# Optimization experiments

Measured on AMD Instinct MI355X. Metric: run time of the kernel, lower is better.

## Reference

```python
import jax, jax.numpy as jnp
import numpy as np

BITS_W = 2  # WAGE default weight bitwidth


def _scale(bits):
    return 2.0 ** (bits - 1)


def quantize_w(x):
    """WAGE Quantize.W: clip to [-1+delta, 1-delta], round to grid of step delta,
    with straight-through estimator for gradients."""
    s = _scale(BITS_W)
    delta = 1.0 / s
    xc = jnp.clip(x, -1.0 + delta, 1.0 - delta)
    y = jnp.round(xc * s) / s
    # straight-through: forward uses y, gradient flows as identity to x
    return x + jax.lax.stop_gradient(y - x)


def setup_inputs() -> dict:
    key = jax.random.key(0)
    k1, k2 = jax.random.split(key)
    B, D_IN, C_OUT = 16384, 1024, 1024
    inputs = jax.random.normal(k1, (B, D_IN), dtype=jnp.float32)
    # learned kernel per build(): shape [d_in, c_out]
    kernel = jax.random.normal(k2, (D_IN, C_OUT), dtype=jnp.float32) * 0.5
    return {"inputs": inputs, "kernel": kernel}


def reference(inputs, kernel):
    # quantize weights every forward pass, then dense matmul
    return jnp.matmul(inputs, quantize_w(kernel))
```

## Files before the change

kernel.cpp:

```cpp
#include <hip/hip_runtime.h>

typedef unsigned short u16;
typedef unsigned int u32;

typedef __bf16 bf16x8 __attribute__((ext_vector_type(8)));
typedef float floatx4 __attribute__((ext_vector_type(4)));


__device__ __forceinline__ u32 f2bf(float f) {
    u32 u = __builtin_bit_cast(u32, f);
    return (u + 0x7fffu + ((u >> 16) & 1u)) >> 16;
}

__device__ __forceinline__ float quant_w(float x) {
    float xc = fminf(fmaxf(x, -0.5f), 0.5f);
    return rintf(xc * 2.0f) * 0.5f;
}

__device__ __forceinline__ void gload_lds16(const u16* g, u16* l) {
    __builtin_amdgcn_global_load_lds(
        (const __attribute__((address_space(1))) void*)g,
        (__attribute__((address_space(3))) void*)l,
        16, 0, 0);
}


__global__ __launch_bounds__(256) void cast_a_kernel(const float4* __restrict__ in,
                                                     uint4* __restrict__ out) {
    int t = blockIdx.x * 256 + threadIdx.x;
    float4 a = in[2 * t];
    float4 b = in[2 * t + 1];
    uint4 o;
    o.x = f2bf(a.x) | (f2bf(a.y) << 16);
    o.y = f2bf(a.z) | (f2bf(a.w) << 16);
    o.z = f2bf(b.x) | (f2bf(b.y) << 16);
    o.w = f2bf(b.z) | (f2bf(b.w) << 16);
    out[t] = o;
}


__global__ __launch_bounds__(256) void quant_transpose_kernel(const float* __restrict__ W,
                                                              u16* __restrict__ Bt) {
    __shared__ u16 tile[32][33];
    const int KN = 1024;
    int tx = threadIdx.x;
    int ty = threadIdx.y;
    int k0 = blockIdx.y * 32;
    int n0 = blockIdx.x * 32;
#pragma unroll
    for (int i = 0; i < 4; i++) {
        int kl = ty + i * 8;
        float x = W[(k0 + kl) * KN + n0 + tx];
        tile[kl][tx] = (u16)f2bf(quant_w(x));
    }
    __syncthreads();
#pragma unroll
    for (int i = 0; i < 4; i++) {
        int nl = ty + i * 8;
        Bt[(n0 + nl) * KN + k0 + tx] = tile[tx][nl];
    }
}


__global__ __launch_bounds__(256) void gemm_bt_kernel(const u16* __restrict__ A,
                                                      const u16* __restrict__ Bt,
                                                      float* __restrict__ C) {
    const int K = 1024;
    const int N = 1024;

    __shared__ alignas(16) u16 As[128 * 64];
    __shared__ alignas(16) u16 Bs[128 * 64];

    const int tid = threadIdx.x;
    const int mbase = blockIdx.x * 128;
    const int nbase = blockIdx.y * 128;
    const int lane = tid & 63;
    const int wv = tid >> 6;
    const int wm = (wv & 1) * 64;
    const int wn = (wv >> 1) * 64;
    const int frow = lane & 15;
    const int fkc = lane >> 4;
    const int rsw = frow & 7;

    floatx4 acc[4][4] = {};

    const int srow = tid >> 3;
    const int g8 = (tid & 7) ^ (srow & 7);
    const u16* Aga[4];
    const u16* Bga[4];
#pragma unroll
    for (int q = 0; q < 4; q++) {
        Aga[q] = &A[(size_t)(mbase + q * 32 + srow) * K + g8 * 8];
        Bga[q] = &Bt[(size_t)(nbase + q * 32 + srow) * K + g8 * 8];
    }

    for (int kt = 0; kt < K; kt += 64) {
        __syncthreads();
#pragma unroll
        for (int q = 0; q < 4; q++) {
            gload_lds16(Aga[q] + kt, &As[(q * 256 + tid) * 8]);
            gload_lds16(Bga[q] + kt, &Bs[(q * 256 + tid) * 8]);
        }
        __syncthreads();

#pragma unroll
        for (int s = 0; s < 2; s++) {
            bf16x8 af[4], bf[4];
#pragma unroll
            for (int i = 0; i < 4; i++)
                af[i] = *(const bf16x8*)&As[(wm + i * 16 + frow) * 64 +
                                            (((s * 4 + fkc) ^ rsw) * 8)];
#pragma unroll
            for (int j = 0; j < 4; j++)
                bf[j] = *(const bf16x8*)&Bs[(wn + j * 16 + frow) * 64 +
                                            (((s * 4 + fkc) ^ rsw) * 8)];
#pragma unroll
            for (int i = 0; i < 4; i++)
#pragma unroll
                for (int j = 0; j < 4; j++)
                    acc[i][j] = __builtin_amdgcn_mfma_f32_16x16x32_bf16(
                        af[i], bf[j], acc[i][j], 0, 0, 0);
        }
    }

    const int crow = (lane >> 4) * 4;
    const int ccol = lane & 15;
#pragma unroll
    for (int i = 0; i < 4; i++) {
#pragma unroll
        for (int j = 0; j < 4; j++) {
            float* cp = &C[(size_t)(mbase + wm + i * 16 + crow) * N + nbase + wn + j * 16 + ccol];
#pragma unroll
            for (int r = 0; r < 4; r++) cp[r * N] = acc[i][j][r];
        }
    }
}


extern "C" void kernel_launch(void* const* d_in, const int* in_sizes, int n_in,
                              void* d_out, int out_size, void* d_ws, size_t ws_size,
                              hipStream_t stream) {
    const float* A = (const float*)d_in[0];
    const float* W = (const float*)d_in[1];
    float* C = (float*)d_out;

    u16* Abf = (u16*)d_ws;
    u16* Btq = (u16*)((char*)d_ws + (size_t)33554432);

    cast_a_kernel<<<8192, 256, 0, stream>>>((const float4*)A, (uint4*)Abf);
    quant_transpose_kernel<<<dim3(32, 32), dim3(32, 8), 0, stream>>>(W, Btq);
    gemm_bt_kernel<<<dim3(128, 8), 256, 0, stream>>>(Abf, Btq, C);
}
```

Before: 151.0 us.

## Fuse fp32-to-bf16 cast of A into GEMM tile load

Drops the separate cast kernel that wrote a bf16 copy of A. The GEMM now reads fp32 A directly, converts it with a packed bf16 convert instruction, and writes the swizzled LDS tile through registers. This removes a launch plus the write and re-read of a 32 MB intermediate. In exchange A is loaded synchronously through VGPRs rather than asynchronously into LDS, and each A element is re-read and re-converted by all 8 N-blocks, doubling A traffic from L2/HBM.

```diff
diff --git a/kernel.cpp b/kernel.cpp
--- a/kernel.cpp
+++ b/kernel.cpp
@@ -17,25 +17,17 @@
     return rintf(xc * 2.0f) * 0.5f;
 }
 
+__device__ __forceinline__ u32 cvt_pk_bf16(float lo, float hi) {
+    u32 r;
+    asm("v_cvt_pk_bf16_f32 %0, %1, %2" : "=v"(r) : "v"(lo), "v"(hi));
+    return r;
+}
+
 __device__ __forceinline__ void gload_lds16(const u16* g, u16* l) {
     __builtin_amdgcn_global_load_lds(
         (const __attribute__((address_space(1))) void*)g,
         (__attribute__((address_space(3))) void*)l,
         16, 0, 0);
-}
-
-
-__global__ __launch_bounds__(256) void cast_a_kernel(const float4* __restrict__ in,
-                                                     uint4* __restrict__ out) {
-    int t = blockIdx.x * 256 + threadIdx.x;
-    float4 a = in[2 * t];
-    float4 b = in[2 * t + 1];
-    uint4 o;
-    o.x = f2bf(a.x) | (f2bf(a.y) << 16);
-    o.y = f2bf(a.z) | (f2bf(a.w) << 16);
-    o.z = f2bf(b.x) | (f2bf(b.y) << 16);
-    o.w = f2bf(b.z) | (f2bf(b.w) << 16);
-    out[t] = o;
 }
 
 
@@ -62,9 +54,9 @@
 }
 
 
-__global__ __launch_bounds__(256) void gemm_bt_kernel(const u16* __restrict__ A,
-                                                      const u16* __restrict__ Bt,
-                                                      float* __restrict__ C) {
+__global__ __launch_bounds__(256) void gemm_fused_kernel(const float* __restrict__ A32,
+                                                         const u16* __restrict__ Bt,
+                                                         float* __restrict__ C) {
     const int K = 1024;
     const int N = 1024;
 
@@ -86,21 +78,40 @@
 
     const int srow = tid >> 3;
     const int g8 = (tid & 7) ^ (srow & 7);
-    const u16* Aga[4];
     const u16* Bga[4];
 #pragma unroll
-    for (int q = 0; q < 4; q++) {
-        Aga[q] = &A[(size_t)(mbase + q * 32 + srow) * K + g8 * 8];
+    for (int q = 0; q < 4; q++)
         Bga[q] = &Bt[(size_t)(nbase + q * 32 + srow) * K + g8 * 8];
-    }
+
+    const int ar = tid >> 1;
+    const int ah = tid & 1;
+    const float* Ag = &A32[(size_t)(mbase + ar) * K + ah * 32];
+    u16* Aw[4];
+#pragma unroll
+    for (int c = 0; c < 4; c++)
+        Aw[c] = &As[ar * 64 + (((ah * 4 + c) ^ (ar & 7)) * 8)];
 
     for (int kt = 0; kt < K; kt += 64) {
         __syncthreads();
+
 #pragma unroll
-        for (int q = 0; q < 4; q++) {
-            gload_lds16(Aga[q] + kt, &As[(q * 256 + tid) * 8]);
+        for (int q = 0; q < 4; q++)
             gload_lds16(Bga[q] + kt, &Bs[(q * 256 + tid) * 8]);
+
+        float4 av[8];
+#pragma unroll
+        for (int i = 0; i < 8; i++)
+            av[i] = *(const float4*)&Ag[kt + 4 * i];
+#pragma unroll
+        for (int c = 0; c < 4; c++) {
+            uint4 w;
+            w.x = cvt_pk_bf16(av[2 * c].x, av[2 * c].y);
+            w.y = cvt_pk_bf16(av[2 * c].z, av[2 * c].w);
+            w.z = cvt_pk_bf16(av[2 * c + 1].x, av[2 * c + 1].y);
+            w.w = cvt_pk_bf16(av[2 * c + 1].z, av[2 * c + 1].w);
+            *(uint4*)Aw[c] = w;
         }
+
         __syncthreads();
 
 #pragma unroll
@@ -144,10 +155,8 @@
     const float* W = (const float*)d_in[1];
     float* C = (float*)d_out;
 
-    u16* Abf = (u16*)d_ws;
-    u16* Btq = (u16*)((char*)d_ws + (size_t)33554432);
+    u16* Btq = (u16*)d_ws;
 
-    cast_a_kernel<<<8192, 256, 0, stream>>>((const float4*)A, (uint4*)Abf);
     quant_transpose_kernel<<<dim3(32, 32), dim3(32, 8), 0, stream>>>(W, Btq);
-    gemm_bt_kernel<<<dim3(128, 8), 256, 0, stream>>>(Abf, Btq, C);
+    gemm_fused_kernel<<<dim3(128, 8), 256, 0, stream>>>(A, Btq, C);
 }
```

New measurement: 182.8 us. 21.1% more time.

## Rewrite GEMM as 256x256-tile 8-wave kernel with double-buffered phased prefetch

Applied to the files above, without the earlier changes.

Replaces the 128x128 single-buffered GEMM with a 256x256 tile per 512-thread block. LDS is double-buffered across k-steps, and the global-to-LDS loads are split into quarter stages interleaved with four MFMA phases per k-step. Explicit vmcnt waits, barriers and setprio are used to overlap memory traffic with compute. It aims to hide load latency and raise data reuse per tile, at the cost of much higher register and LDS use (128KB) and a grid of only 256 blocks.

```diff
diff --git a/kernel.cpp b/kernel.cpp
--- a/kernel.cpp
+++ b/kernel.cpp
@@ -62,74 +62,161 @@
 }
 
 
-__global__ __launch_bounds__(256) void gemm_bt_kernel(const u16* __restrict__ A,
-                                                      const u16* __restrict__ Bt,
-                                                      float* __restrict__ C) {
+__global__ __launch_bounds__(512, 2) void gemm_8phase_kernel(const u16* __restrict__ A,
+                                                             const u16* __restrict__ Bt,
+                                                             float* __restrict__ C) {
     const int K = 1024;
     const int N = 1024;
 
-    __shared__ alignas(16) u16 As[128 * 64];
-    __shared__ alignas(16) u16 Bs[128 * 64];
+    __shared__ alignas(16) u16 As[2 * 2 * 128 * 64];
+    __shared__ alignas(16) u16 Bs[2 * 2 * 128 * 64];
 
     const int tid = threadIdx.x;
-    const int mbase = blockIdx.x * 128;
-    const int nbase = blockIdx.y * 128;
     const int lane = tid & 63;
-    const int wv = tid >> 6;
-    const int wm = (wv & 1) * 64;
-    const int wn = (wv >> 1) * 64;
+    const int wid = tid >> 6;
+    const int wm = wid >> 2;
+    const int wn = wid & 3;
     const int frow = lane & 15;
     const int fkc = lane >> 4;
     const int rsw = frow & 7;
-
-    floatx4 acc[4][4] = {};
-
-    const int srow = tid >> 3;
-    const int g8 = (tid & 7) ^ (srow & 7);
-    const u16* Aga[4];
-    const u16* Bga[4];
-#pragma unroll
-    for (int q = 0; q < 4; q++) {
-        Aga[q] = &A[(size_t)(mbase + q * 32 + srow) * K + g8 * 8];
-        Bga[q] = &Bt[(size_t)(nbase + q * 32 + srow) * K + g8 * 8];
-    }
-
-    for (int kt = 0; kt < K; kt += 64) {
-        __syncthreads();
-#pragma unroll
-        for (int q = 0; q < 4; q++) {
-            gload_lds16(Aga[q] + kt, &As[(q * 256 + tid) * 8]);
-            gload_lds16(Bga[q] + kt, &Bs[(q * 256 + tid) * 8]);
+    const int mbase = blockIdx.x * 256;
+    const int nbase = blockIdx.y * 256;
+
+    const int sr = tid >> 3;
+    const int gc = (tid & 7) ^ (sr & 7);
+
+    const u16* Abase = &A[(size_t)(mbase + sr) * K + gc * 8];
+    const u16* Bbase = &Bt[(size_t)(nbase + sr) * K + gc * 8];
+
+    floatx4 acc[8][4] = {};
+
+    auto stage = [&](int tau, int q) {
+        const int hf = q & 1;
+        const int isA = q >> 1;
+        const u16* gb = isA ? Abase : Bbase;
+        u16* lb = isA ? As : Bs;
+        const size_t goff = (size_t)(hf * 128) * K + (size_t)tau * 64;
+        u16* dst = &lb[(((tau & 1) * 2 + hf) * 8192) + tid * 8];
+        gload_lds16(gb + goff, dst);
+        gload_lds16(gb + goff + (size_t)64 * K, dst + 4096);
+    };
+
+#define BAR_PRE()                              \
+    __builtin_amdgcn_sched_barrier(0);         \
+    __builtin_amdgcn_s_barrier();              \
+    __builtin_amdgcn_sched_barrier(0);         \
+    __builtin_amdgcn_s_setprio(1)
+#define BAR_POST()                             \
+    __builtin_amdgcn_s_setprio(0);             \
+    __builtin_amdgcn_sched_barrier(0);         \
+    __builtin_amdgcn_s_barrier();              \
+    __builtin_amdgcn_sched_barrier(0)
+
+    stage(0, 0); stage(0, 1); stage(0, 2); stage(0, 3);
+    asm volatile("s_waitcnt vmcnt(4)" ::: "memory");
+    stage(1, 0); stage(1, 1); stage(1, 2);
+    asm volatile("s_waitcnt vmcnt(6)" ::: "memory");
+    __builtin_amdgcn_sched_barrier(0);
+    __builtin_amdgcn_s_barrier();
+    __builtin_amdgcn_sched_barrier(0);
+
+    for (int t = 0; t < 16; t++) {
+        const int b = t & 1;
+        const int a_sl = ((b * 2 + wm) * 128) * 64;
+        const int b_sl = ((b * 2 + (wn >> 1)) * 128) * 64;
+        const int lrb0 = (wn & 1) * 64;
+
+        bf16x8 af0[4][2], af1[4][2], bf0[2][2], bf1[2][2];
+
+#pragma unroll
+        for (int mf = 0; mf < 4; mf++)
+#pragma unroll
+            for (int s = 0; s < 2; s++)
+                af0[mf][s] = *(const bf16x8*)&As[a_sl + (mf * 16 + frow) * 64 +
+                                                (((s * 4 + fkc) ^ rsw) * 8)];
+#pragma unroll
+        for (int nf = 0; nf < 2; nf++)
+#pragma unroll
+            for (int s = 0; s < 2; s++)
+                bf0[nf][s] = *(const bf16x8*)&Bs[b_sl + (lrb0 + nf * 16 + frow) * 64 +
+                                                 (((s * 4 + fkc) ^ rsw) * 8)];
+        if (t < 15) stage(t + 1, 3);
+        BAR_PRE();
+#pragma unroll
+        for (int mf = 0; mf < 4; mf++)
+#pragma unroll
+            for (int nf = 0; nf < 2; nf++)
+#pragma unroll
+                for (int s = 0; s < 2; s++)
+                    acc[mf][nf] = __builtin_amdgcn_mfma_f32_16x16x32_bf16(
+                        af0[mf][s], bf0[nf][s], acc[mf][nf], 0, 0, 0);
+        BAR_POST();
+
+#pragma unroll
+        for (int nf = 0; nf < 2; nf++)
+#pragma unroll
+            for (int s = 0; s < 2; s++)
+                bf1[nf][s] = *(const bf16x8*)&Bs[b_sl + (lrb0 + 32 + nf * 16 + frow) * 64 +
+                                                 (((s * 4 + fkc) ^ rsw) * 8)];
+        if (t < 14) stage(t + 2, 0);
+        BAR_PRE();
+#pragma unroll
+        for (int mf = 0; mf < 4; mf++)
+#pragma unroll
+            for (int nf = 0; nf < 2; nf++)
+#pragma unroll
+                for (int s = 0; s < 2; s++)
+                    acc[mf][2 + nf] = __builtin_amdgcn_mfma_f32_16x16x32_bf16(
+                        af0[mf][s], bf1[nf][s], acc[mf][2 + nf], 0, 0, 0);
+        BAR_POST();
+
+#pragma unroll
+        for (int mf = 0; mf < 4; mf++)
+#pragma unroll
+            for (int s = 0; s < 2; s++)
+                af1[mf][s] = *(const bf16x8*)&As[a_sl + (64 + mf * 16 + frow) * 64 +
+                                                (((s * 4 + fkc) ^ rsw) * 8)];
+        if (t < 14) stage(t + 2, 1);
+        BAR_PRE();
+#pragma unroll
+        for (int mf = 0; mf < 4; mf++)
+#pragma unroll
+            for (int nf = 0; nf < 2; nf++)
+#pragma unroll
+                for (int s = 0; s < 2; s++)
+                    acc[4 + mf][nf] = __builtin_amdgcn_mfma_f32_16x16x32_bf16(
+                        af1[mf][s], bf0[nf][s], acc[4 + mf][nf], 0, 0, 0);
+        BAR_POST();
+
+        if (t < 14) stage(t + 2, 2);
+        if (t < 14) {
+            asm volatile("s_waitcnt vmcnt(6)" ::: "memory");
+        } else if (t == 14) {
+            asm volatile("s_waitcnt vmcnt(0)" ::: "memory");
         }
-        __syncthreads();
-
-#pragma unroll
-        for (int s = 0; s < 2; s++) {
-            bf16x8 af[4], bf[4];
-#pragma unroll
-            for (int i = 0; i < 4; i++)
-                af[i] = *(const bf16x8*)&As[(wm + i * 16 + frow) * 64 +
-                                            (((s * 4 + fkc) ^ rsw) * 8)];
-#pragma unroll
-            for (int j = 0; j < 4; j++)
-                bf[j] = *(const bf16x8*)&Bs[(wn + j * 16 + frow) * 64 +
-                                            (((s * 4 + fkc) ^ rsw) * 8)];
-#pragma unroll
-            for (int i = 0; i < 4; i++)
-#pragma unroll
-                for (int j = 0; j < 4; j++)
-                    acc[i][j] = __builtin_amdgcn_mfma_f32_16x16x32_bf16(
-                        af[i], bf[j], acc[i][j], 0, 0, 0);
-        }
-    }
+        BAR_PRE();
+#pragma unroll
+        for (int mf = 0; mf < 4; mf++)
+#pragma unroll
+            for (int nf = 0; nf < 2; nf++)
+#pragma unroll
+                for (int s = 0; s < 2; s++)
+                    acc[4 + mf][2 + nf] = __builtin_amdgcn_mfma_f32_16x16x32_bf16(
+                        af1[mf][s], bf1[nf][s], acc[4 + mf][2 + nf], 0, 0, 0);
+        BAR_POST();
+    }
+
+#undef BAR_PRE
+#undef BAR_POST
 
     const int crow = (lane >> 4) * 4;
     const int ccol = lane & 15;
 #pragma unroll
-    for (int i = 0; i < 4; i++) {
+    for (int i = 0; i < 8; i++) {
 #pragma unroll
         for (int j = 0; j < 4; j++) {
-            float* cp = &C[(size_t)(mbase + wm + i * 16 + crow) * N + nbase + wn + j * 16 + ccol];
+            float* cp = &C[(size_t)(mbase + wm * 128 + i * 16 + crow) * N +
+                           nbase + wn * 64 + j * 16 + ccol];
 #pragma unroll
             for (int r = 0; r < 4; r++) cp[r * N] = acc[i][j][r];
         }
@@ -149,5 +236,5 @@
 
     cast_a_kernel<<<8192, 256, 0, stream>>>((const float4*)A, (uint4*)Abf);
     quant_transpose_kernel<<<dim3(32, 32), dim3(32, 8), 0, stream>>>(W, Btq);
-    gemm_bt_kernel<<<dim3(128, 8), 256, 0, stream>>>(Abf, Btq, C);
-}
+    gemm_8phase_kernel<<<dim3(64, 4), 512, 0, stream>>>(Abf, Btq, C);
+}
```

Result: no change. 150.4 us (-0.4%).

## Rewrite GEMM as 256x256 tile, 8-wave, double-buffered pipelined kernel

Applied to the files above, without the earlier changes.

Replaces the 128x128 single-buffered bf16 GEMM with a 256x256 tile per block using 8 waves and double-buffered LDS. Global-to-LDS loads for tile t+2 are issued while MFMAs run on the current tile, and LDS fragment reads are interleaved with MFMA clusters, using explicit waitcnt, barriers and setprio. The goal is to hide memory latency and raise data reuse per block. In exchange it uses 128KB of LDS and more registers per block, and the grid shrinks to 256 blocks, which may underfill the GPU's CUs.

```diff
diff --git a/kernel.cpp b/kernel.cpp
--- a/kernel.cpp
+++ b/kernel.cpp
@@ -62,74 +62,136 @@
 }
 
 
-__global__ __launch_bounds__(256) void gemm_bt_kernel(const u16* __restrict__ A,
-                                                      const u16* __restrict__ Bt,
-                                                      float* __restrict__ C) {
+__global__ __launch_bounds__(512, 2) void gemm_4region_kernel(const u16* __restrict__ A,
+                                                              const u16* __restrict__ Bt,
+                                                              float* __restrict__ C) {
     const int K = 1024;
     const int N = 1024;
 
-    __shared__ alignas(16) u16 As[128 * 64];
-    __shared__ alignas(16) u16 Bs[128 * 64];
+    __shared__ alignas(16) u16 As[2 * 2 * 128 * 64];
+    __shared__ alignas(16) u16 Bs[2 * 2 * 128 * 64];
 
     const int tid = threadIdx.x;
-    const int mbase = blockIdx.x * 128;
-    const int nbase = blockIdx.y * 128;
     const int lane = tid & 63;
-    const int wv = tid >> 6;
-    const int wm = (wv & 1) * 64;
-    const int wn = (wv >> 1) * 64;
+    const int wid = tid >> 6;
+    const int wm = wid >> 2;
+    const int wn = wid & 3;
     const int frow = lane & 15;
     const int fkc = lane >> 4;
     const int rsw = frow & 7;
-
-    floatx4 acc[4][4] = {};
-
-    const int srow = tid >> 3;
-    const int g8 = (tid & 7) ^ (srow & 7);
-    const u16* Aga[4];
-    const u16* Bga[4];
-#pragma unroll
-    for (int q = 0; q < 4; q++) {
-        Aga[q] = &A[(size_t)(mbase + q * 32 + srow) * K + g8 * 8];
-        Bga[q] = &Bt[(size_t)(nbase + q * 32 + srow) * K + g8 * 8];
-    }
-
-    for (int kt = 0; kt < K; kt += 64) {
-        __syncthreads();
-#pragma unroll
-        for (int q = 0; q < 4; q++) {
-            gload_lds16(Aga[q] + kt, &As[(q * 256 + tid) * 8]);
-            gload_lds16(Bga[q] + kt, &Bs[(q * 256 + tid) * 8]);
+    const int mbase = blockIdx.x * 256;
+    const int nbase = blockIdx.y * 256;
+
+    const int sr = tid >> 3;
+    const int gc = (tid & 7) ^ (sr & 7);
+
+    const u16* Abase = &A[(size_t)(mbase + sr) * K + gc * 8];
+    const u16* Bbase = &Bt[(size_t)(nbase + sr) * K + gc * 8];
+
+    floatx4 acc[8][4] = {};
+    bf16x8 af0[4][2], af1[4][2], bf0[2][2], bf1[2][2];
+
+    auto stage = [&](int tau, int q) {
+        const int hf = q & 1;
+        const int isA = q >> 1;
+        const u16* gb = isA ? Abase : Bbase;
+        u16* lb = isA ? As : Bs;
+        const size_t goff = (size_t)(hf * 128) * K + (size_t)tau * 64;
+        u16* dst = &lb[(((tau & 1) * 2 + hf) * 8192) + tid * 8];
+        gload_lds16(gb + goff, dst);
+        gload_lds16(gb + goff + (size_t)64 * K, dst + 4096);
+    };
+
+#define LGKM0() asm volatile("s_waitcnt lgkmcnt(0)" ::: "memory")
+#define VMC(n)  asm volatile("s_waitcnt vmcnt(" #n ")" ::: "memory")
+#define BAR()                          \
+    __builtin_amdgcn_sched_barrier(0); \
+    __builtin_amdgcn_s_barrier();      \
+    __builtin_amdgcn_sched_barrier(0)
+
+#define READ_AF0(b)                                                                  \
+    _Pragma("unroll") for (int mf = 0; mf < 4; mf++)                                 \
+        _Pragma("unroll") for (int s = 0; s < 2; s++)                                \
+            af0[mf][s] = *(const bf16x8*)&As[(((b)*2 + wm) * 128 + mf * 16 + frow) * 64 + \
+                                             (((s * 4 + fkc) ^ rsw) * 8)]
+#define READ_AF1(b)                                                                  \
+    _Pragma("unroll") for (int mf = 0; mf < 4; mf++)                                 \
+        _Pragma("unroll") for (int s = 0; s < 2; s++)                                \
+            af1[mf][s] = *(const bf16x8*)&As[(((b)*2 + wm) * 128 + 64 + mf * 16 + frow) * 64 + \
+                                             (((s * 4 + fkc) ^ rsw) * 8)]
+#define READ_BF0(b)                                                                  \
+    _Pragma("unroll") for (int nf = 0; nf < 2; nf++)                                 \
+        _Pragma("unroll") for (int s = 0; s < 2; s++)                                \
+            bf0[nf][s] = *(const bf16x8*)&Bs[(((b)*2 + (wn >> 1)) * 128 + (wn & 1) * 64 + nf * 16 + frow) * 64 + \
+                                             (((s * 4 + fkc) ^ rsw) * 8)]
+#define READ_BF1(b)                                                                  \
+    _Pragma("unroll") for (int nf = 0; nf < 2; nf++)                                 \
+        _Pragma("unroll") for (int s = 0; s < 2; s++)                                \
+            bf1[nf][s] = *(const bf16x8*)&Bs[(((b)*2 + (wn >> 1)) * 128 + (wn & 1) * 64 + 32 + nf * 16 + frow) * 64 + \
+                                             (((s * 4 + fkc) ^ rsw) * 8)]
+#define MFMA_CL(af, bf, mo, no)                                                      \
+    __builtin_amdgcn_s_setprio(1);                                                   \
+    _Pragma("unroll") for (int mf = 0; mf < 4; mf++)                                 \
+        _Pragma("unroll") for (int nf = 0; nf < 2; nf++)                             \
+            _Pragma("unroll") for (int s = 0; s < 2; s++)                            \
+                acc[(mo) + mf][(no) + nf] = __builtin_amdgcn_mfma_f32_16x16x32_bf16( \
+                    af[mf][s], bf[nf][s], acc[(mo) + mf][(no) + nf], 0, 0, 0);       \
+    __builtin_amdgcn_s_setprio(0)
+
+    stage(0, 0); stage(0, 1); stage(0, 2); stage(0, 3);
+    stage(1, 0); stage(1, 1); stage(1, 2); stage(1, 3);
+    VMC(8);
+    BAR();
+
+    for (int t = 0; t < 16; t++) {
+        const int b = t & 1;
+
+        if (t > 0) { MFMA_CL(af1, bf1, 4, 2); }
+        READ_AF0(b);
+        READ_BF0(b);
+        LGKM0();
+        BAR();
+
+        MFMA_CL(af0, bf0, 0, 0);
+        READ_AF1(b);
+        LGKM0();
+        BAR();
+
+        MFMA_CL(af1, bf0, 4, 0);
+        READ_BF1(b);
+        if (t <= 13) { stage(t + 2, 2); stage(t + 2, 3); }
+        LGKM0();
+        BAR();
+
+        MFMA_CL(af0, bf1, 0, 2);
+        if (t <= 13) {
+            stage(t + 2, 0); stage(t + 2, 1);
+            VMC(8);
+        } else if (t == 14) {
+            VMC(0);
         }
-        __syncthreads();
-
-#pragma unroll
-        for (int s = 0; s < 2; s++) {
-            bf16x8 af[4], bf[4];
-#pragma unroll
-            for (int i = 0; i < 4; i++)
-                af[i] = *(const bf16x8*)&As[(wm + i * 16 + frow) * 64 +
-                                            (((s * 4 + fkc) ^ rsw) * 8)];
-#pragma unroll
-            for (int j = 0; j < 4; j++)
-                bf[j] = *(const bf16x8*)&Bs[(wn + j * 16 + frow) * 64 +
-                                            (((s * 4 + fkc) ^ rsw) * 8)];
-#pragma unroll
-            for (int i = 0; i < 4; i++)
-#pragma unroll
-                for (int j = 0; j < 4; j++)
-                    acc[i][j] = __builtin_amdgcn_mfma_f32_16x16x32_bf16(
-                        af[i], bf[j], acc[i][j], 0, 0, 0);
-        }
-    }
+        BAR();
+    }
+
+    MFMA_CL(af1, bf1, 4, 2);
+
+#undef LGKM0
+#undef VMC
+#undef BAR
+#undef READ_AF0
+#undef READ_AF1
+#undef READ_BF0
+#undef READ_BF1
+#undef MFMA_CL
 
     const int crow = (lane >> 4) * 4;
     const int ccol = lane & 15;
 #pragma unroll
-    for (int i = 0; i < 4; i++) {
+    for (int i = 0; i < 8; i++) {
 #pragma unroll
         for (int j = 0; j < 4; j++) {
-            float* cp = &C[(size_t)(mbase + wm + i * 16 + crow) * N + nbase + wn + j * 16 + ccol];
+            float* cp = &C[(size_t)(mbase + wm * 128 + i * 16 + crow) * N +
+                           nbase + wn * 64 + j * 16 + ccol];
 #pragma unroll
             for (int r = 0; r < 4; r++) cp[r * N] = acc[i][j][r];
         }
@@ -149,5 +211,5 @@
 
     cast_a_kernel<<<8192, 256, 0, stream>>>((const float4*)A, (uint4*)Abf);
     quant_transpose_kernel<<<dim3(32, 32), dim3(32, 8), 0, stream>>>(W, Btq);
-    gemm_bt_kernel<<<dim3(128, 8), 256, 0, stream>>>(Abf, Btq, C);
-}
+    gemm_4region_kernel<<<dim3(64, 4), 512, 0, stream>>>(Abf, Btq, C);
+}
```

Measured after the change: 145.2 us. 3.9% less time.
